# Optimization experiments

Measured on AMD Instinct MI355X. Metric: run time of the kernel, lower is better.

## Reference

```python
import jax, jax.numpy as jnp
import numpy as np

B, N, DIM, HEADS = 4, 1024, 768, 12
HIDDEN, E, TOPK = 3072, 8, 2
EPS = 1e-5  # nn.LayerNorm default


def _layernorm(x, g, b):
    mu = jnp.mean(x, axis=-1, keepdims=True)
    var = jnp.var(x, axis=-1, keepdims=True)
    return (x - mu) * jax.lax.rsqrt(var + EPS) * g + b


def setup_inputs() -> dict:
    key = jax.random.key(0)
    ks = jax.random.split(key, 10)
    s = 0.02
    return {
        "x": jax.random.normal(ks[0], (B, N, DIM), dtype=jnp.float32),
        "ln1_g": jnp.ones((DIM,), jnp.float32),
        "ln1_b": jnp.zeros((DIM,), jnp.float32),
        "qkv_w": jax.random.normal(ks[1], (3 * DIM, DIM), jnp.float32) * s,  # qkv_bias=False
        "proj_w": jax.random.normal(ks[2], (DIM, DIM), jnp.float32) * s,
        "proj_b": jnp.zeros((DIM,), jnp.float32),
        "ln2_g": jnp.ones((DIM,), jnp.float32),
        "ln2_b": jnp.zeros((DIM,), jnp.float32),
        "gate_w": jax.random.normal(ks[3], (E, DIM), jnp.float32) * s,
        "gate_b": jnp.zeros((E,), jnp.float32),
        "w1": jax.random.normal(ks[4], (E, HIDDEN, DIM), jnp.float32) * s,
        "b1": jnp.zeros((E, HIDDEN), jnp.float32),
        "w2": jax.random.normal(ks[5], (E, DIM, HIDDEN), jnp.float32) * s,
        "b2": jnp.zeros((E, DIM), jnp.float32),
    }


def reference(x, ln1_g, ln1_b, qkv_w, proj_w, proj_b, ln2_g, ln2_b,
              gate_w, gate_b, w1, b1, w2, b2):
    b, n, d = x.shape
    hd = d // HEADS
    scale = hd ** -0.5

    # ---- attention branch ----
    h = _layernorm(x, ln1_g, ln1_b)
    qkv = h @ qkv_w.T                                   # [B,N,3D]
    qkv = qkv.reshape(b, n, 3, HEADS, hd).transpose(2, 0, 3, 1, 4)
    q, k, v = qkv[0], qkv[1], qkv[2]                    # [B,H,N,hd]
    attn = jax.nn.softmax(jnp.einsum('bhnd,bhmd->bhnm', q, k) * scale, axis=-1)
    a = jnp.einsum('bhnm,bhmd->bhnd', attn, v)
    a = a.transpose(0, 2, 1, 3).reshape(b, n, d)
    a = a @ proj_w.T + proj_b
    x = x + a

    # ---- MoE branch (NaiveGate, top_k=2) ----
    h2 = _layernorm(x, ln2_g, ln2_b)
    t = h2.reshape(-1, d)                               # [T,D]
    T = t.shape[0]
    logits = t @ gate_w.T + gate_b                      # [T,E]
    top_val, top_idx = jax.lax.top_k(logits, TOPK)
    score = jax.nn.softmax(top_val, axis=-1)            # softmax over top-k logits
    # per-token combine weight for each expert, [T,E]
    cw = jnp.zeros((T, E), t.dtype).at[jnp.arange(T)[:, None], top_idx].add(score)

    out = jnp.zeros_like(t)
    for e in range(E):  # small fixed expert count; exact (no capacity drop)
        he = jax.nn.gelu(t @ w1[e].T + b1[e], approximate=False)
        ye = he @ w2[e].T + b2[e]
        out = out + cw[:, e:e + 1] * ye

    return x + out.reshape(b, n, d)
```

## Files before the change

kernel.cpp:

```cpp
#include <hip/hip_runtime.h>
#include <math.h>

typedef short s16x8 __attribute__((ext_vector_type(8)));
typedef float f32x4 __attribute__((ext_vector_type(4)));
typedef unsigned short u16x4 __attribute__((ext_vector_type(4)));
typedef unsigned short u16x8 __attribute__((ext_vector_type(8)));

#define DIM_ 768
#define HID_ 3072
#define NTOK 4096
#define CAP 9216

__device__ __forceinline__ unsigned short f2bf(float f) {
  unsigned u = __float_as_uint(f);
  u += 0x7fffu + ((u >> 16) & 1u);
  return (unsigned short)(u >> 16);
}
__device__ __forceinline__ float bf2f(unsigned short u) {
  return __uint_as_float(((unsigned)u) << 16);
}

__device__ __forceinline__ void async_cp16(const void* g, void* l) {
  __builtin_amdgcn_global_load_lds(
      (const __attribute__((address_space(1))) void*)g,
      (__attribute__((address_space(3))) void*)l, 16, 0, 0);
}

template<bool BBF>
__device__ __forceinline__ void gemm_loop(
    const unsigned short* aS0, const unsigned short* aS1,
    const void* __restrict__ Bv, int ldb,
    int kbeg, int kend, int col0,
    unsigned short* lA, unsigned short* lB,
    f32x4 acc[4][4])
{
  const int tid = threadIdx.x;
  const int lane = tid & 63;
  const int w = tid >> 6;
  const int wm = (w >> 1) << 6;
  const int wn = (w & 1) << 6;
  const int g = lane >> 4;
  const int lm = lane & 15;

  if constexpr (BBF) {
    const unsigned short* Bb = (const unsigned short*)Bv;
    const unsigned short* bS[2];
#pragma unroll
    for (int it = 0; it < 2; ++it) {
      int c = (w * 2 + it) * 64 + lane;
      int r = c >> 2, ks = ((c & 3) ^ ((r >> 1) & 3)) << 3;
      bS[it] = Bb + (size_t)(col0 + r) * ldb + ks;
    }
    auto stage = [&](int k0, int p) {
      async_cp16(aS0 + k0, lA + p * 4096 + (w * 2 + 0) * 512);
      async_cp16(bS[0] + k0, lB + p * 4096 + (w * 2 + 0) * 512);
      async_cp16(aS1 + k0, lA + p * 4096 + (w * 2 + 1) * 512);
      async_cp16(bS[1] + k0, lB + p * 4096 + (w * 2 + 1) * 512);
    };
    stage(kbeg, 0);
    int p = 0;
    for (int k0 = kbeg; k0 < kend; k0 += 32) {
      __syncthreads();
      if (k0 + 32 < kend) stage(k0 + 32, p ^ 1);
      const unsigned short* bA = lA + p * 4096;
      const unsigned short* bB = lB + p * 4096;
      s16x8 a_frag[4], b_frag[4];
#pragma unroll
      for (int mt = 0; mt < 4; ++mt) {
        int ra = wm + mt * 16 + lm;
        a_frag[mt] = *(const s16x8*)(bA + ra * 32 + ((g ^ ((ra >> 1) & 3)) << 3));
      }
#pragma unroll
      for (int nt = 0; nt < 4; ++nt) {
        int cb = wn + nt * 16 + lm;
        b_frag[nt] = *(const s16x8*)(bB + cb * 32 + ((g ^ ((cb >> 1) & 3)) << 3));
      }
#pragma unroll
      for (int mt = 0; mt < 4; ++mt)
#pragma unroll
        for (int nt = 0; nt < 4; ++nt)
          acc[mt][nt] = __builtin_amdgcn_mfma_f32_16x16x32_bf16(
              a_frag[mt], b_frag[nt], acc[mt][nt], 0, 0, 0);
      p ^= 1;
    }
  } else {
    const float* Bf = (const float*)Bv;
    for (int k0 = kbeg; k0 < kend; k0 += 32) {
      __syncthreads();
      async_cp16(aS0 + k0, lA + (w * 2 + 0) * 512);
      async_cp16(aS1 + k0, lA + (w * 2 + 1) * 512);
#pragma unroll
      for (int it = 0; it < 4; ++it) {
        int f = it * 1024 + tid * 4;
        int br = f >> 5, ke = f & 31;
        const float4 vv = *(const float4*)(Bf + (size_t)(col0 + br) * ldb + (k0 + ke));
        u16x4 pk;
        pk[0] = f2bf(vv.x); pk[1] = f2bf(vv.y); pk[2] = f2bf(vv.z); pk[3] = f2bf(vv.w);
        int ksw = (((ke >> 3) ^ ((br >> 1) & 3)) << 3) + (ke & 7);
        *(u16x4*)(lB + br * 32 + ksw) = pk;
      }
      __syncthreads();
      s16x8 a_frag[4], b_frag[4];
#pragma unroll
      for (int mt = 0; mt < 4; ++mt) {
        int ra = wm + mt * 16 + lm;
        a_frag[mt] = *(const s16x8*)(lA + ra * 32 + ((g ^ ((ra >> 1) & 3)) << 3));
      }
#pragma unroll
      for (int nt = 0; nt < 4; ++nt) {
        int cb = wn + nt * 16 + lm;
        b_frag[nt] = *(const s16x8*)(lB + cb * 32 + ((g ^ ((cb >> 1) & 3)) << 3));
      }
#pragma unroll
      for (int mt = 0; mt < 4; ++mt)
#pragma unroll
        for (int nt = 0; nt < 4; ++nt)
          acc[mt][nt] = __builtin_amdgcn_mfma_f32_16x16x32_bf16(
              a_frag[mt], b_frag[nt], acc[mt][nt], 0, 0, 0);
    }
  }
}

#define GEMM_PROLOGUE                                   \
  __shared__ unsigned short lA[8192];                   \
  __shared__ unsigned short lB[8192];                   \
  f32x4 acc[4][4];                                      \
  _Pragma("unroll") for (int a_ = 0; a_ < 4; ++a_)      \
  _Pragma("unroll") for (int b_ = 0; b_ < 4; ++b_) {    \
    acc[a_][b_][0]=0.f; acc[a_][b_][1]=0.f;             \
    acc[a_][b_][2]=0.f; acc[a_][b_][3]=0.f; }           \
  const int lane = threadIdx.x & 63;                    \
  const int w = threadIdx.x >> 6;                       \
  const int wm = (w >> 1) << 6, wn = (w & 1) << 6;      \
  const int g = lane >> 4, lm = lane & 15;

#define A_PTRS(Abase, LDA)                                            \
  const unsigned short* aS[2];                                        \
  _Pragma("unroll") for (int it_ = 0; it_ < 2; ++it_) {               \
    int c_ = (w * 2 + it_) * 64 + lane;                               \
    int r_ = c_ >> 2, ks_ = ((c_ & 3) ^ ((r_ >> 1) & 3)) << 3;        \
    aS[it_] = (Abase) + (size_t)(row0 + r_) * (LDA) + ks_;            \
  }


__global__ void k_cvtln(const float* __restrict__ s0, const float* __restrict__ s1,
                        const float* __restrict__ s2, const float* __restrict__ s3,
                        unsigned short* __restrict__ d0, unsigned short* __restrict__ d1,
                        unsigned short* __restrict__ d2, unsigned short* __restrict__ d3,
                        int ncvt,
                        const float* __restrict__ x, const float* __restrict__ gg,
                        const float* __restrict__ bb, unsigned short* __restrict__ outb)
{
  __shared__ float red[8];
  if ((int)blockIdx.x < ncvt) {
    long i = (long)(blockIdx.x * 256 + threadIdx.x) * 8;
    const float* s; unsigned short* d;
    if (i < 1769472)             { s = s0;            d = d0; }
    else if (i < 2359296)        { s = s1 - 1769472;  d = d1 - 1769472; }
    else if (i < 21233664)       { s = s2 - 2359296;  d = d2 - 2359296; }
    else                         { s = s3 - 21233664; d = d3 - 21233664; }
    float4 a = *(const float4*)(s + i);
    float4 b = *(const float4*)(s + i + 4);
    u16x8 o;
    o[0]=f2bf(a.x); o[1]=f2bf(a.y); o[2]=f2bf(a.z); o[3]=f2bf(a.w);
    o[4]=f2bf(b.x); o[5]=f2bf(b.y); o[6]=f2bf(b.z); o[7]=f2bf(b.w);
    *(u16x8*)(d + i) = o;
    return;
  }
  int t = blockIdx.x - ncvt, tid = threadIdx.x;
  const float* xr = x + (size_t)t * DIM_;
  float v0 = xr[tid], v1 = xr[tid + 256], v2 = xr[tid + 512];
  float s = v0 + v1 + v2, q = v0 * v0 + v1 * v1 + v2 * v2;
  for (int o = 32; o; o >>= 1) { s += __shfl_xor(s, o, 64); q += __shfl_xor(q, o, 64); }
  int lane = tid & 63, w = tid >> 6;
  if (!lane) { red[w] = s; red[4 + w] = q; }
  __syncthreads();
  s = red[0] + red[1] + red[2] + red[3];
  q = red[4] + red[5] + red[6] + red[7];
  float mean = s * (1.f / 768.f);
  float rstd = rsqrtf(q * (1.f / 768.f) - mean * mean + 1e-5f);
  unsigned short* orow = outb + (size_t)t * DIM_;
  orow[tid]       = f2bf((v0 - mean) * rstd * gg[tid]       + bb[tid]);
  orow[tid + 256] = f2bf((v1 - mean) * rstd * gg[tid + 256] + bb[tid + 256]);
  orow[tid + 512] = f2bf((v2 - mean) * rstd * gg[tid + 512] + bb[tid + 512]);
}

template<bool BBF>
__global__ __launch_bounds__(256, 2) void k_qkv(
    const unsigned short* __restrict__ hbf, const void* __restrict__ qkvw,
    unsigned short* __restrict__ qkvb)
{
  GEMM_PROLOGUE
  int f = blockIdx.x, xcd = f & 7, s = f >> 3;
  int cg = s / 24, rr = (s % 24) / 6, c = cg * 6 + s % 6;
  int row0 = (xcd * 4 + rr) * 128, col0 = c * 128;
  A_PTRS(hbf, DIM_)
  gemm_loop<BBF>(aS[0], aS[1], qkvw, DIM_, 0, DIM_, col0, lA, lB, acc);
#pragma unroll
  for (int mt = 0; mt < 4; ++mt)
#pragma unroll
    for (int nt = 0; nt < 4; ++nt)
#pragma unroll
      for (int i = 0; i < 4; ++i) {
        int m = row0 + wm + mt * 16 + g * 4 + i;
        int n = col0 + wn + nt * 16 + lm;
        int which = (n >= 1536) ? 2 : (n >= 768 ? 1 : 0);
        int d = n - which * 768;
        int head = d >> 6, hd = d & 63;
        int b = m >> 10, nn = m & 1023;
        int bh = b * 12 + head;
        size_t addr = (which < 2)
            ? ((size_t)which * 3145728u + (size_t)bh * 65536u + (size_t)nn * 64 + hd)
            : (6291456u + (size_t)bh * 65536u + (size_t)hd * 1024 + nn);
        qkvb[addr] = f2bf(acc[mt][nt][i]);
      }
}

__global__ __launch_bounds__(256, 2) void k_attn(
    const unsigned short* __restrict__ qkv, unsigned short* __restrict__ abuf)
{
  __shared__ unsigned short lK[2][4096];
  __shared__ unsigned short lV[2][4096];
  __shared__ unsigned short lP[4][16 * 72];
  const int tid = threadIdx.x, lane = tid & 63, w = tid >> 6;
  const int g = lane >> 4, lm = lane & 15;
  const int f = blockIdx.x, xcd = f & 7, s = f >> 3;
  const int bh = xcd * 6 + (s >> 4);
  const int qt = s & 15;
  const unsigned short* qsec = qkv + (size_t)bh * 65536u;
  const unsigned short* ksec = qkv + 3145728u + (size_t)bh * 65536u;
  const unsigned short* vsec = qkv + 6291456u + (size_t)bh * 65536u;

  s16x8 bq[2];
  {
    const unsigned short* qp = qsec + (size_t)(qt * 64 + w * 16 + lm) * 64 + g * 8;
    bq[0] = *(const s16x8*)(qp);
    bq[1] = *(const s16x8*)(qp + 32);
  }
  f32x4 oacc[4];
#pragma unroll
  for (int dt = 0; dt < 4; ++dt) { oacc[dt][0]=0.f; oacc[dt][1]=0.f; oacc[dt][2]=0.f; oacc[dt][3]=0.f; }
  float m_i = -3.0e38f, l_i = 0.f;

  auto stage = [&](int kt, int p) {
#pragma unroll
    for (int it = 0; it < 2; ++it) {
      int c = (w * 2 + it) * 64 + lane;
      int r = c >> 3, sl = (c & 7) ^ (r & 7);
      async_cp16(ksec + (size_t)(kt * 64 + r) * 64 + sl * 8, lK[p] + (w * 2 + it) * 512);
      async_cp16(vsec + (size_t)r * 1024 + kt * 64 + sl * 8, lV[p] + (w * 2 + it) * 512);
    }
  };
  stage(0, 0);
  int p = 0;
  for (int kt = 0; kt < 16; ++kt) {
    __syncthreads();
    if (kt < 15) stage(kt + 1, p ^ 1);
    f32x4 st[4];
#pragma unroll
    for (int mt = 0; mt < 4; ++mt) {
      f32x4 z; z[0]=0.f; z[1]=0.f; z[2]=0.f; z[3]=0.f;
#pragma unroll
      for (int ks = 0; ks < 2; ++ks) {
        int ra = mt * 16 + lm;
        s16x8 a = *(const s16x8*)(lK[p] + ra * 64 + (((ks * 4 + g) ^ (ra & 7)) << 3));
        z = __builtin_amdgcn_mfma_f32_16x16x32_bf16(a, bq[ks], z, 0, 0, 0);
      }
      st[mt] = z;
    }
    float mx = -3.0e38f;
#pragma unroll
    for (int mt = 0; mt < 4; ++mt) {
      st[mt] *= 0.125f;
#pragma unroll
      for (int i = 0; i < 4; ++i) mx = fmaxf(mx, st[mt][i]);
    }
    mx = fmaxf(mx, __shfl_xor(mx, 16, 64));
    mx = fmaxf(mx, __shfl_xor(mx, 32, 64));
    float mnew = fmaxf(m_i, mx);
    float alpha = expf(m_i - mnew);
    float psum = 0.f;
#pragma unroll
    for (int mt = 0; mt < 4; ++mt) {
      u16x4 pk;
#pragma unroll
      for (int i = 0; i < 4; ++i) {
        float p2 = expf(st[mt][i] - mnew);
        psum += p2;
        pk[i] = f2bf(p2);
      }
      *(u16x4*)(&lP[w][lm * 72 + mt * 16 + g * 4]) = pk;
    }
    psum += __shfl_xor(psum, 16, 64);
    psum += __shfl_xor(psum, 32, 64);
    l_i = l_i * alpha + psum;
    m_i = mnew;
    float al[4];
#pragma unroll
    for (int i = 0; i < 4; ++i) al[i] = __shfl(alpha, (lane & 48) | (g * 4 + i), 64);
#pragma unroll
    for (int dt = 0; dt < 4; ++dt) {
#pragma unroll
      for (int i = 0; i < 4; ++i) oacc[dt][i] *= al[i];
    }
#pragma unroll
    for (int ks = 0; ks < 2; ++ks) {
      s16x8 ap = *(const s16x8*)(&lP[w][lm * 72 + ks * 32 + g * 8]);
#pragma unroll
      for (int dt = 0; dt < 4; ++dt) {
        int rv = dt * 16 + lm;
        s16x8 bv = *(const s16x8*)(lV[p] + rv * 64 + (((ks * 4 + g) ^ (rv & 7)) << 3));
        oacc[dt] = __builtin_amdgcn_mfma_f32_16x16x32_bf16(ap, bv, oacc[dt], 0, 0, 0);
      }
    }
    p ^= 1;
  }
  float linv[4];
#pragma unroll
  for (int i = 0; i < 4; ++i)
    linv[i] = 1.f / __shfl(l_i, (lane & 48) | (g * 4 + i), 64);
  int b = bh / 12, head = bh % 12;
#pragma unroll
  for (int dt = 0; dt < 4; ++dt)
#pragma unroll
    for (int i = 0; i < 4; ++i) {
      int q = qt * 64 + w * 16 + g * 4 + i;
      int col = head * 64 + dt * 16 + lm;
      abuf[(size_t)(b * 1024 + q) * DIM_ + col] = f2bf(oacc[dt][i] * linv[i]);
    }
}

template<bool BBF>
__global__ __launch_bounds__(256, 2) void k_proj(
    const unsigned short* __restrict__ abuf, const void* __restrict__ projw,
    const float* __restrict__ projb, const float* __restrict__ x,
    float* __restrict__ x1)
{
  GEMM_PROLOGUE
  int row0 = blockIdx.x * 128, col0 = blockIdx.y * 128;
  A_PTRS(abuf, DIM_)
  gemm_loop<BBF>(aS[0], aS[1], projw, DIM_, 0, DIM_, col0, lA, lB, acc);
#pragma unroll
  for (int mt = 0; mt < 4; ++mt)
#pragma unroll
    for (int nt = 0; nt < 4; ++nt)
#pragma unroll
      for (int i = 0; i < 4; ++i) {
        int m = row0 + wm + mt * 16 + g * 4 + i;
        int n = col0 + wn + nt * 16 + lm;
        size_t idx = (size_t)m * DIM_ + n;
        x1[idx] = acc[mt][nt][i] + projb[n] + x[idx];
      }
}

template<bool BBF>
__global__ __launch_bounds__(256, 2) void k_ffn1(
    const unsigned short* __restrict__ h2, const void* __restrict__ w1,
    const float* __restrict__ b1, const int* __restrict__ off,
    const int* __restrict__ tok_of, const unsigned short* __restrict__ zrow,
    unsigned short* __restrict__ hidden)
{
  int f = blockIdx.x, xcd = f & 7, s = f >> 3;
  int cg = s / 72, rr = (s % 72) >> 3, c = cg * 8 + (s & 7);
  int row0 = (xcd * 9 + rr) * 128, col0 = c * 128;
  if (row0 >= off[8]) return;
  int e = 0;
  while (!(row0 >= off[e] && row0 < off[e + 1])) ++e;
  GEMM_PROLOGUE
  const unsigned short* aS[2];
#pragma unroll
  for (int it = 0; it < 2; ++it) {
    int cc = (w * 2 + it) * 64 + lane;
    int r = cc >> 2, ks = ((cc & 3) ^ ((r >> 1) & 3)) << 3;
    int tk = tok_of[row0 + r];
    const unsigned short* rp = (tk >= 0) ? (h2 + (size_t)tk * DIM_) : zrow;
    aS[it] = rp + ks;
  }
  const char* Bp = (const char*)w1 + (size_t)e * HID_ * DIM_ * (BBF ? 2 : 4);
  gemm_loop<BBF>(aS[0], aS[1], Bp, DIM_, 0, DIM_, col0, lA, lB, acc);
#pragma unroll
  for (int mt = 0; mt < 4; ++mt)
#pragma unroll
    for (int nt = 0; nt < 4; ++nt)
#pragma unroll
      for (int i = 0; i < 4; ++i) {
        int m = row0 + wm + mt * 16 + g * 4 + i;
        int n = col0 + wn + nt * 16 + lm;
        float v = acc[mt][nt][i] + b1[e * HID_ + n];
        float ge = 0.5f * v * (1.f + erff(v * 0.70710678118654752f));
        hidden[(size_t)m * HID_ + n] = f2bf(ge);
      }
}

template<bool BBF>
__global__ __launch_bounds__(256, 2) void k_ffn2(
    const unsigned short* __restrict__ hidden, const void* __restrict__ w2,
    const float* __restrict__ b2, const int* __restrict__ off,
    unsigned short* __restrict__ ye0, unsigned short* __restrict__ ye1)
{
  int f = blockIdx.x, xcd = f & 7, s = f >> 3;
  int cg = s / 54, rem = s % 54;
  int rr = rem / 6, kk = (rem % 6) / 3, c = cg * 3 + rem % 3;
  int row0 = (xcd * 9 + rr) * 128, col0 = c * 128;
  if (row0 >= off[8]) return;
  int e = 0;
  while (!(row0 >= off[e] && row0 < off[e + 1])) ++e;
  GEMM_PROLOGUE
  A_PTRS(hidden, HID_)
  const char* Bp = (const char*)w2 + (size_t)e * DIM_ * HID_ * (BBF ? 2 : 4);
  gemm_loop<BBF>(aS[0], aS[1], Bp, HID_, kk * 1536, kk * 1536 + 1536, col0, lA, lB, acc);
  unsigned short* yh = kk ? ye1 : ye0;
#pragma unroll
  for (int mt = 0; mt < 4; ++mt)
#pragma unroll
    for (int nt = 0; nt < 4; ++nt)
#pragma unroll
      for (int i = 0; i < 4; ++i) {
        int m = row0 + wm + mt * 16 + g * 4 + i;
        int n = col0 + wn + nt * 16 + lm;
        float v = acc[mt][nt][i] + (kk ? 0.f : b2[e * DIM_ + n]);
        yh[(size_t)m * DIM_ + n] = f2bf(v);
      }
}

__global__ __launch_bounds__(256) void k_ln2gate(
    const float* __restrict__ x1, const float* __restrict__ gg,
    const float* __restrict__ bb, const float* __restrict__ gw,
    const float* __restrict__ gb, unsigned short* __restrict__ h2,
    int* __restrict__ topidx, float* __restrict__ tops)
{
  int t = blockIdx.x, tid = threadIdx.x;
  const float* xr = x1 + (size_t)t * DIM_;
  float v0 = xr[tid], v1 = xr[tid + 256], v2 = xr[tid + 512];
  float s = v0 + v1 + v2, q = v0 * v0 + v1 * v1 + v2 * v2;
  for (int o = 32; o; o >>= 1) { s += __shfl_xor(s, o, 64); q += __shfl_xor(q, o, 64); }
  __shared__ float red[8];
  __shared__ float part[32];
  int lane = tid & 63, w = tid >> 6;
  if (!lane) { red[w] = s; red[4 + w] = q; }
  __syncthreads();
  s = red[0] + red[1] + red[2] + red[3];
  q = red[4] + red[5] + red[6] + red[7];
  float mean = s * (1.f / 768.f);
  float rstd = rsqrtf(q * (1.f / 768.f) - mean * mean + 1e-5f);
  float y0 = (v0 - mean) * rstd * gg[tid]       + bb[tid];
  float y1 = (v1 - mean) * rstd * gg[tid + 256] + bb[tid + 256];
  float y2 = (v2 - mean) * rstd * gg[tid + 512] + bb[tid + 512];
  unsigned short* hrow = h2 + (size_t)t * DIM_;
  hrow[tid] = f2bf(y0); hrow[tid + 256] = f2bf(y1); hrow[tid + 512] = f2bf(y2);
#pragma unroll
  for (int e = 0; e < 8; ++e) {
    float p = y0 * gw[e * DIM_ + tid] + y1 * gw[e * DIM_ + tid + 256] + y2 * gw[e * DIM_ + tid + 512];
    for (int o = 32; o; o >>= 1) p += __shfl_xor(p, o, 64);
    if (!lane) part[e * 4 + w] = p;
  }
  __syncthreads();
  if (tid == 0) {
    float lg[8];
#pragma unroll
    for (int e = 0; e < 8; ++e)
      lg[e] = part[e * 4] + part[e * 4 + 1] + part[e * 4 + 2] + part[e * 4 + 3] + gb[e];
    int i0 = 0; float b0 = lg[0];
#pragma unroll
    for (int e = 1; e < 8; ++e) if (lg[e] > b0) { b0 = lg[e]; i0 = e; }
    int i1 = (i0 == 0) ? 1 : 0; float b1v = lg[i1];
#pragma unroll
    for (int e = 0; e < 8; ++e)
      if (e != i0 && lg[e] > b1v) { b1v = lg[e]; i1 = e; }
    float e1 = expf(b1v - b0);
    float s0 = 1.f / (1.f + e1);
    topidx[t * 2] = i0; topidx[t * 2 + 1] = i1;
    tops[t * 2] = s0;  tops[t * 2 + 1] = e1 / (1.f + e1);
  }
}

__global__ __launch_bounds__(1024) void k_route(
    const int* __restrict__ topidx, int* __restrict__ pos_of, int* __restrict__ off,
    int* __restrict__ tok_of, unsigned short* __restrict__ zrow)
{
  __shared__ int scnt[8], soff[9], sfill[8];
  int tid = threadIdx.x;
  if (tid < 8) { scnt[tid] = 0; sfill[tid] = 0; }
  if (tid < 384) ((unsigned*)zrow)[tid] = 0;
  for (int j = tid; j < CAP; j += 1024) tok_of[j] = -1;
  __syncthreads();
#pragma unroll
  for (int j = 0; j < 8; ++j)
    atomicAdd(&scnt[topidx[tid + j * 1024]], 1);
  __syncthreads();
  if (tid == 0) {
    int a = 0;
    for (int e = 0; e < 8; ++e) { soff[e] = a; off[e] = a; a += (scnt[e] + 127) & ~127; }
    soff[8] = a; off[8] = a;
  }
  __syncthreads();
#pragma unroll
  for (int j = 0; j < 8; ++j) {
    int i = tid + j * 1024;
    int e = topidx[i];
    int p = soff[e] + atomicAdd(&sfill[e], 1);
    pos_of[i] = p;
    tok_of[p] = i >> 1;
  }
}

__global__ void k_combine(const float* __restrict__ x1,
                          const unsigned short* __restrict__ y0h,
                          const unsigned short* __restrict__ y1h,
                          const int* __restrict__ pos_of, const float* __restrict__ tops,
                          float* __restrict__ out) {
  int t = blockIdx.x, tid = threadIdx.x;
  int p0 = pos_of[t * 2], p1 = pos_of[t * 2 + 1];
  float s0 = tops[t * 2], s1 = tops[t * 2 + 1];
  const float* xr = x1 + (size_t)t * DIM_;
  const unsigned short* a0 = y0h + (size_t)p0 * DIM_;
  const unsigned short* a1 = y1h + (size_t)p0 * DIM_;
  const unsigned short* b0 = y0h + (size_t)p1 * DIM_;
  const unsigned short* b1 = y1h + (size_t)p1 * DIM_;
  float* orow = out + (size_t)t * DIM_;
#pragma unroll
  for (int j = 0; j < 3; ++j) {
    int col = tid + j * 256;
    float ya = bf2f(a0[col]) + bf2f(a1[col]);
    float yb = bf2f(b0[col]) + bf2f(b1[col]);
    orow[col] = xr[col] + s0 * ya + s1 * yb;
  }
}

extern "C" void kernel_launch(void* const* d_in, const int* in_sizes, int n_in,
                              void* d_out, int out_size, void* d_ws, size_t ws_size,
                              hipStream_t stream) {
  const float* x     = (const float*)d_in[0];
  const float* ln1g  = (const float*)d_in[1];
  const float* ln1b  = (const float*)d_in[2];
  const float* qkvw  = (const float*)d_in[3];
  const float* projw = (const float*)d_in[4];
  const float* projb = (const float*)d_in[5];
  const float* ln2g  = (const float*)d_in[6];
  const float* ln2b  = (const float*)d_in[7];
  const float* gw    = (const float*)d_in[8];
  const float* gb    = (const float*)d_in[9];
  const float* w1    = (const float*)d_in[10];
  const float* b1    = (const float*)d_in[11];
  const float* w2    = (const float*)d_in[12];
  const float* b2    = (const float*)d_in[13];
  float* out = (float*)d_out;

  char* base = (char*)d_ws;
  unsigned short* hbf    = (unsigned short*)(base + 0);
  unsigned short* qkvb   = (unsigned short*)(base + 6291456);
  unsigned short* abuf   = (unsigned short*)(base + 25165824);
  float*          x1     = (float*)(base + 31457280);
  unsigned short* hidden = (unsigned short*)(base + 44040192);
  unsigned short* ye0    = (unsigned short*)(base + 100663296);
  unsigned short* ye1    = (unsigned short*)(base + 114819072);

  const size_t FULL_NEED = 209190912;
  const bool full = ws_size >= FULL_NEED;
  unsigned short *wqkvbf, *wprojbf, *w1bf = nullptr, *w2bf = nullptr;
  if (full) {
    wqkvbf  = (unsigned short*)(base + 128974848);
    wprojbf = (unsigned short*)(base + 132513792);
    w1bf    = (unsigned short*)(base + 133693440);
    w2bf    = (unsigned short*)(base + 171442176);
  } else {
    wqkvbf  = (unsigned short*)(base + 44040192);
    wprojbf = (unsigned short*)(base + 44040192 + 3538944);
  }
  char* small = base + 25165824;
  int*   topidx = (int*)small;
  float* tops   = (float*)(small + 32768);
  int*   pos_of = (int*)(small + 65536);
  int*   off    = (int*)(small + 98304);
  int*   tok_of = (int*)(small + 98368);
  unsigned short* zrow = (unsigned short*)(small + 135232);
  unsigned short* h2 = hbf;

  int ncvt = full ? 19584 : 1152;
  k_cvtln<<<ncvt + NTOK, 256, 0, stream>>>(qkvw, projw, w1, w2,
                                           wqkvbf, wprojbf, w1bf, w2bf,
                                           ncvt, x, ln1g, ln1b, hbf);
  k_qkv<true><<<576, 256, 0, stream>>>(hbf, wqkvbf, qkvb);
  k_attn<<<768, 256, 0, stream>>>(qkvb, abuf);
  k_proj<true><<<dim3(32, 6), 256, 0, stream>>>(abuf, wprojbf, projb, x, x1);
  k_ln2gate<<<NTOK, 256, 0, stream>>>(x1, ln2g, ln2b, gw, gb, h2, topidx, tops);
  k_route<<<1, 1024, 0, stream>>>(topidx, pos_of, off, tok_of, zrow);
  if (full) {
    k_ffn1<true><<<1728, 256, 0, stream>>>(h2, w1bf, b1, off, tok_of, zrow, hidden);
    k_ffn2<true><<<864, 256, 0, stream>>>(hidden, w2bf, b2, off, ye0, ye1);
  } else {
    k_ffn1<false><<<1728, 256, 0, stream>>>(h2, w1, b1, off, tok_of, zrow, hidden);
    k_ffn2<false><<<864, 256, 0, stream>>>(hidden, w2, b2, off, ye0, ye1);
  }
  k_combine<<<NTOK, 256, 0, stream>>>(x1, ye0, ye1, pos_of, tops, out);
}
```

Baseline: 481.0 us.

## Fuse MoE combine into ffn2 via atomics and overlap weight conversion with QKV

```diff
diff --git a/kernel.cpp b/kernel.cpp
--- a/kernel.cpp
+++ b/kernel.cpp
@@ -24,6 +24,16 @@
   __builtin_amdgcn_global_load_lds(
       (const __attribute__((address_space(1))) void*)g,
       (__attribute__((address_space(3))) void*)l, 16, 0, 0);
+}
+
+__device__ __forceinline__ void cvt2048(const float* __restrict__ s,
+                                        unsigned short* __restrict__ d, long i) {
+  float4 a = *(const float4*)(s + i);
+  float4 b = *(const float4*)(s + i + 4);
+  u16x8 o;
+  o[0]=f2bf(a.x); o[1]=f2bf(a.y); o[2]=f2bf(a.z); o[3]=f2bf(a.w);
+  o[4]=f2bf(b.x); o[5]=f2bf(b.y); o[6]=f2bf(b.z); o[7]=f2bf(b.w);
+  *(u16x8*)(d + i) = o;
 }
 
 template<bool BBF>
@@ -144,30 +154,18 @@
 
 
 __global__ void k_cvtln(const float* __restrict__ s0, const float* __restrict__ s1,
-                        const float* __restrict__ s2, const float* __restrict__ s3,
                         unsigned short* __restrict__ d0, unsigned short* __restrict__ d1,
-                        unsigned short* __restrict__ d2, unsigned short* __restrict__ d3,
-                        int ncvt,
                         const float* __restrict__ x, const float* __restrict__ gg,
                         const float* __restrict__ bb, unsigned short* __restrict__ outb)
 {
   __shared__ float red[8];
-  if ((int)blockIdx.x < ncvt) {
+  if ((int)blockIdx.x < 1152) {
     long i = (long)(blockIdx.x * 256 + threadIdx.x) * 8;
-    const float* s; unsigned short* d;
-    if (i < 1769472)             { s = s0;            d = d0; }
-    else if (i < 2359296)        { s = s1 - 1769472;  d = d1 - 1769472; }
-    else if (i < 21233664)       { s = s2 - 2359296;  d = d2 - 2359296; }
-    else                         { s = s3 - 21233664; d = d3 - 21233664; }
-    float4 a = *(const float4*)(s + i);
-    float4 b = *(const float4*)(s + i + 4);
-    u16x8 o;
-    o[0]=f2bf(a.x); o[1]=f2bf(a.y); o[2]=f2bf(a.z); o[3]=f2bf(a.w);
-    o[4]=f2bf(b.x); o[5]=f2bf(b.y); o[6]=f2bf(b.z); o[7]=f2bf(b.w);
-    *(u16x8*)(d + i) = o;
+    if (i < 1769472) cvt2048(s0, d0, i);
+    else             cvt2048(s1 - 1769472, d1 - 1769472, i);
     return;
   }
-  int t = blockIdx.x - ncvt, tid = threadIdx.x;
+  int t = blockIdx.x - 1152, tid = threadIdx.x;
   const float* xr = x + (size_t)t * DIM_;
   float v0 = xr[tid], v1 = xr[tid + 256], v2 = xr[tid + 512];
   float s = v0 + v1 + v2, q = v0 * v0 + v1 * v1 + v2 * v2;
@@ -185,17 +183,27 @@
   orow[tid + 512] = f2bf((v2 - mean) * rstd * gg[tid + 512] + bb[tid + 512]);
 }
 
-template<bool BBF>
-__global__ __launch_bounds__(256, 2) void k_qkv(
+template<bool FULL>
+__global__ __launch_bounds__(256, 4) void k_qkvcvt(
     const unsigned short* __restrict__ hbf, const void* __restrict__ qkvw,
-    unsigned short* __restrict__ qkvb)
+    unsigned short* __restrict__ qkvb,
+    const float* __restrict__ w1f, const float* __restrict__ w2f,
+    unsigned short* __restrict__ w1bf, unsigned short* __restrict__ w2bf)
 {
   GEMM_PROLOGUE
+  if constexpr (FULL) {
+    if ((int)blockIdx.x >= 576) {
+      int c2 = blockIdx.x - 576;
+      if (c2 < 9216) cvt2048(w1f, w1bf, (long)c2 * 2048 + threadIdx.x * 8);
+      else           cvt2048(w2f, w2bf, (long)(c2 - 9216) * 2048 + threadIdx.x * 8);
+      return;
+    }
+  }
   int f = blockIdx.x, xcd = f & 7, s = f >> 3;
   int cg = s / 24, rr = (s % 24) / 6, c = cg * 6 + s % 6;
   int row0 = (xcd * 4 + rr) * 128, col0 = c * 128;
   A_PTRS(hbf, DIM_)
-  gemm_loop<BBF>(aS[0], aS[1], qkvw, DIM_, 0, DIM_, col0, lA, lB, acc);
+  gemm_loop<true>(aS[0], aS[1], qkvw, DIM_, 0, DIM_, col0, lA, lB, acc);
 #pragma unroll
   for (int mt = 0; mt < 4; ++mt)
 #pragma unroll
@@ -330,8 +338,7 @@
     }
 }
 
-template<bool BBF>
-__global__ __launch_bounds__(256, 2) void k_proj(
+__global__ __launch_bounds__(256, 4) void k_proj(
     const unsigned short* __restrict__ abuf, const void* __restrict__ projw,
     const float* __restrict__ projb, const float* __restrict__ x,
     float* __restrict__ x1)
@@ -339,7 +346,7 @@
   GEMM_PROLOGUE
   int row0 = blockIdx.x * 128, col0 = blockIdx.y * 128;
   A_PTRS(abuf, DIM_)
-  gemm_loop<BBF>(aS[0], aS[1], projw, DIM_, 0, DIM_, col0, lA, lB, acc);
+  gemm_loop<true>(aS[0], aS[1], projw, DIM_, 0, DIM_, col0, lA, lB, acc);
 #pragma unroll
   for (int mt = 0; mt < 4; ++mt)
 #pragma unroll
@@ -354,7 +361,7 @@
 }
 
 template<bool BBF>
-__global__ __launch_bounds__(256, 2) void k_ffn1(
+__global__ __launch_bounds__(256, 4) void k_ffn1(
     const unsigned short* __restrict__ h2, const void* __restrict__ w1,
     const float* __restrict__ b1, const int* __restrict__ off,
     const int* __restrict__ tok_of, const unsigned short* __restrict__ zrow,
@@ -393,10 +400,11 @@
 }
 
 template<bool BBF>
-__global__ __launch_bounds__(256, 2) void k_ffn2(
+__global__ __launch_bounds__(256, 4) void k_ffn2(
     const unsigned short* __restrict__ hidden, const void* __restrict__ w2,
     const float* __restrict__ b2, const int* __restrict__ off,
-    unsigned short* __restrict__ ye0, unsigned short* __restrict__ ye1)
+    const int* __restrict__ tok_of, const float* __restrict__ cw_of,
+    float* __restrict__ out)
 {
   int f = blockIdx.x, xcd = f & 7, s = f >> 3;
   int cg = s / 54, rem = s % 54;
@@ -409,29 +417,35 @@
   A_PTRS(hidden, HID_)
   const char* Bp = (const char*)w2 + (size_t)e * DIM_ * HID_ * (BBF ? 2 : 4);
   gemm_loop<BBF>(aS[0], aS[1], Bp, HID_, kk * 1536, kk * 1536 + 1536, col0, lA, lB, acc);
-  unsigned short* yh = kk ? ye1 : ye0;
 #pragma unroll
   for (int mt = 0; mt < 4; ++mt)
 #pragma unroll
-    for (int nt = 0; nt < 4; ++nt)
-#pragma unroll
-      for (int i = 0; i < 4; ++i) {
-        int m = row0 + wm + mt * 16 + g * 4 + i;
+    for (int i = 0; i < 4; ++i) {
+      int m = row0 + wm + mt * 16 + g * 4 + i;
+      int tok = tok_of[m];
+      if (tok < 0) continue;
+      float cw = cw_of[m];
+      float* orow = out + (size_t)tok * DIM_;
+#pragma unroll
+      for (int nt = 0; nt < 4; ++nt) {
         int n = col0 + wn + nt * 16 + lm;
         float v = acc[mt][nt][i] + (kk ? 0.f : b2[e * DIM_ + n]);
-        yh[(size_t)m * DIM_ + n] = f2bf(v);
-      }
+        atomicAdd(orow + n, cw * v);
+      }
+    }
 }
 
 __global__ __launch_bounds__(256) void k_ln2gate(
     const float* __restrict__ x1, const float* __restrict__ gg,
     const float* __restrict__ bb, const float* __restrict__ gw,
     const float* __restrict__ gb, unsigned short* __restrict__ h2,
-    int* __restrict__ topidx, float* __restrict__ tops)
+    int* __restrict__ topidx, float* __restrict__ tops, float* __restrict__ out)
 {
   int t = blockIdx.x, tid = threadIdx.x;
   const float* xr = x1 + (size_t)t * DIM_;
   float v0 = xr[tid], v1 = xr[tid + 256], v2 = xr[tid + 512];
+  float* orow = out + (size_t)t * DIM_;
+  orow[tid] = v0; orow[tid + 256] = v1; orow[tid + 512] = v2;
   float s = v0 + v1 + v2, q = v0 * v0 + v1 * v1 + v2 * v2;
   for (int o = 32; o; o >>= 1) { s += __shfl_xor(s, o, 64); q += __shfl_xor(q, o, 64); }
   __shared__ float red[8];
@@ -475,8 +489,9 @@
 }
 
 __global__ __launch_bounds__(1024) void k_route(
-    const int* __restrict__ topidx, int* __restrict__ pos_of, int* __restrict__ off,
-    int* __restrict__ tok_of, unsigned short* __restrict__ zrow)
+    const int* __restrict__ topidx, const float* __restrict__ tops,
+    int* __restrict__ off, int* __restrict__ tok_of, float* __restrict__ cw_of,
+    unsigned short* __restrict__ zrow)
 {
   __shared__ int scnt[8], soff[9], sfill[8];
   int tid = threadIdx.x;
@@ -499,31 +514,8 @@
     int i = tid + j * 1024;
     int e = topidx[i];
     int p = soff[e] + atomicAdd(&sfill[e], 1);
-    pos_of[i] = p;
     tok_of[p] = i >> 1;
-  }
-}
-
-__global__ void k_combine(const float* __restrict__ x1,
-                          const unsigned short* __restrict__ y0h,
-                          const unsigned short* __restrict__ y1h,
-                          const int* __restrict__ pos_of, const float* __restrict__ tops,
-                          float* __restrict__ out) {
-  int t = blockIdx.x, tid = threadIdx.x;
-  int p0 = pos_of[t * 2], p1 = pos_of[t * 2 + 1];
-  float s0 = tops[t * 2], s1 = tops[t * 2 + 1];
-  const float* xr = x1 + (size_t)t * DIM_;
-  const unsigned short* a0 = y0h + (size_t)p0 * DIM_;
-  const unsigned short* a1 = y1h + (size_t)p0 * DIM_;
-  const unsigned short* b0 = y0h + (size_t)p1 * DIM_;
-  const unsigned short* b1 = y1h + (size_t)p1 * DIM_;
-  float* orow = out + (size_t)t * DIM_;
-#pragma unroll
-  for (int j = 0; j < 3; ++j) {
-    int col = tid + j * 256;
-    float ya = bf2f(a0[col]) + bf2f(a1[col]);
-    float yb = bf2f(b0[col]) + bf2f(b1[col]);
-    orow[col] = xr[col] + s0 * ya + s1 * yb;
+    cw_of[p] = tops[i];
   }
 }
 
@@ -552,8 +544,6 @@
   unsigned short* abuf   = (unsigned short*)(base + 25165824);
   float*          x1     = (float*)(base + 31457280);
   unsigned short* hidden = (unsigned short*)(base + 44040192);
-  unsigned short* ye0    = (unsigned short*)(base + 100663296);
-  unsigned short* ye1    = (unsigned short*)(base + 114819072);
 
   const size_t FULL_NEED = 209190912;
   const bool full = ws_size >= FULL_NEED;
@@ -570,27 +560,29 @@
   char* small = base + 25165824;
   int*   topidx = (int*)small;
   float* tops   = (float*)(small + 32768);
-  int*   pos_of = (int*)(small + 65536);
-  int*   off    = (int*)(small + 98304);
-  int*   tok_of = (int*)(small + 98368);
-  unsigned short* zrow = (unsigned short*)(small + 135232);
+  int*   off    = (int*)(small + 65536);
+  int*   tok_of = (int*)(small + 65600);
+  float* cw_of  = (float*)(small + 102464);
+  unsigned short* zrow = (unsigned short*)(small + 139392);
   unsigned short* h2 = hbf;
 
-  int ncvt = full ? 19584 : 1152;
-  k_cvtln<<<ncvt + NTOK, 256, 0, stream>>>(qkvw, projw, w1, w2,
-                                           wqkvbf, wprojbf, w1bf, w2bf,
-                                           ncvt, x, ln1g, ln1b, hbf);
-  k_qkv<true><<<576, 256, 0, stream>>>(hbf, wqkvbf, qkvb);
+  k_cvtln<<<1152 + NTOK, 256, 0, stream>>>(qkvw, projw, wqkvbf, wprojbf,
+                                           x, ln1g, ln1b, hbf);
+  if (full)
+    k_qkvcvt<true><<<576 + 18432, 256, 0, stream>>>(hbf, wqkvbf, qkvb,
+                                                    w1, w2, w1bf, w2bf);
+  else
+    k_qkvcvt<false><<<576, 256, 0, stream>>>(hbf, wqkvbf, qkvb,
+                                             nullptr, nullptr, nullptr, nullptr);
   k_attn<<<768, 256, 0, stream>>>(qkvb, abuf);
-  k_proj<true><<<dim3(32, 6), 256, 0, stream>>>(abuf, wprojbf, projb, x, x1);
-  k_ln2gate<<<NTOK, 256, 0, stream>>>(x1, ln2g, ln2b, gw, gb, h2, topidx, tops);
-  k_route<<<1, 1024, 0, stream>>>(topidx, pos_of, off, tok_of, zrow);
+  k_proj<<<dim3(32, 6), 256, 0, stream>>>(abuf, wprojbf, projb, x, x1);
+  k_ln2gate<<<NTOK, 256, 0, stream>>>(x1, ln2g, ln2b, gw, gb, h2, topidx, tops, out);
+  k_route<<<1, 1024, 0, stream>>>(topidx, tops, off, tok_of, cw_of, zrow);
   if (full) {
     k_ffn1<true><<<1728, 256, 0, stream>>>(h2, w1bf, b1, off, tok_of, zrow, hidden);
-    k_ffn2<true><<<864, 256, 0, stream>>>(hidden, w2bf, b2, off, ye0, ye1);
+    k_ffn2<true><<<864, 256, 0, stream>>>(hidden, w2bf, b2, off, tok_of, cw_of, out);
   } else {
     k_ffn1<false><<<1728, 256, 0, stream>>>(h2, w1, b1, off, tok_of, zrow, hidden);
-    k_ffn2<false><<<864, 256, 0, stream>>>(hidden, w2, b2, off, ye0, ye1);
-  }
-  k_combine<<<NTOK, 256, 0, stream>>>(x1, ye0, ye1, pos_of, tops, out);
-}
+    k_ffn2<false><<<864, 256, 0, stream>>>(hidden, w2, b2, off, tok_of, cw_of, out);
+  }
+}
```

After: 503.2 us. +4.6%, slower.

## Move expert weight conversion into QKV GEMM launch and raise occupancy bounds

Applied to the files above, without the earlier changes.

```diff
diff --git a/kernel.cpp b/kernel.cpp
--- a/kernel.cpp
+++ b/kernel.cpp
@@ -24,6 +24,16 @@
   __builtin_amdgcn_global_load_lds(
       (const __attribute__((address_space(1))) void*)g,
       (__attribute__((address_space(3))) void*)l, 16, 0, 0);
+}
+
+__device__ __forceinline__ void cvt2048(const float* __restrict__ s,
+                                        unsigned short* __restrict__ d, long i) {
+  float4 a = *(const float4*)(s + i);
+  float4 b = *(const float4*)(s + i + 4);
+  u16x8 o;
+  o[0]=f2bf(a.x); o[1]=f2bf(a.y); o[2]=f2bf(a.z); o[3]=f2bf(a.w);
+  o[4]=f2bf(b.x); o[5]=f2bf(b.y); o[6]=f2bf(b.z); o[7]=f2bf(b.w);
+  *(u16x8*)(d + i) = o;
 }
 
 template<bool BBF>
@@ -144,30 +154,18 @@
 
 
 __global__ void k_cvtln(const float* __restrict__ s0, const float* __restrict__ s1,
-                        const float* __restrict__ s2, const float* __restrict__ s3,
                         unsigned short* __restrict__ d0, unsigned short* __restrict__ d1,
-                        unsigned short* __restrict__ d2, unsigned short* __restrict__ d3,
-                        int ncvt,
                         const float* __restrict__ x, const float* __restrict__ gg,
                         const float* __restrict__ bb, unsigned short* __restrict__ outb)
 {
   __shared__ float red[8];
-  if ((int)blockIdx.x < ncvt) {
+  if ((int)blockIdx.x < 1152) {
     long i = (long)(blockIdx.x * 256 + threadIdx.x) * 8;
-    const float* s; unsigned short* d;
-    if (i < 1769472)             { s = s0;            d = d0; }
-    else if (i < 2359296)        { s = s1 - 1769472;  d = d1 - 1769472; }
-    else if (i < 21233664)       { s = s2 - 2359296;  d = d2 - 2359296; }
-    else                         { s = s3 - 21233664; d = d3 - 21233664; }
-    float4 a = *(const float4*)(s + i);
-    float4 b = *(const float4*)(s + i + 4);
-    u16x8 o;
-    o[0]=f2bf(a.x); o[1]=f2bf(a.y); o[2]=f2bf(a.z); o[3]=f2bf(a.w);
-    o[4]=f2bf(b.x); o[5]=f2bf(b.y); o[6]=f2bf(b.z); o[7]=f2bf(b.w);
-    *(u16x8*)(d + i) = o;
+    if (i < 1769472) cvt2048(s0, d0, i);
+    else             cvt2048(s1 - 1769472, d1 - 1769472, i);
     return;
   }
-  int t = blockIdx.x - ncvt, tid = threadIdx.x;
+  int t = blockIdx.x - 1152, tid = threadIdx.x;
   const float* xr = x + (size_t)t * DIM_;
   float v0 = xr[tid], v1 = xr[tid + 256], v2 = xr[tid + 512];
   float s = v0 + v1 + v2, q = v0 * v0 + v1 * v1 + v2 * v2;
@@ -185,17 +183,27 @@
   orow[tid + 512] = f2bf((v2 - mean) * rstd * gg[tid + 512] + bb[tid + 512]);
 }
 
-template<bool BBF>
-__global__ __launch_bounds__(256, 2) void k_qkv(
+template<bool FULL>
+__global__ __launch_bounds__(256, 4) void k_qkvcvt(
     const unsigned short* __restrict__ hbf, const void* __restrict__ qkvw,
-    unsigned short* __restrict__ qkvb)
+    unsigned short* __restrict__ qkvb,
+    const float* __restrict__ w1f, const float* __restrict__ w2f,
+    unsigned short* __restrict__ w1bf, unsigned short* __restrict__ w2bf)
 {
   GEMM_PROLOGUE
+  if constexpr (FULL) {
+    if ((int)blockIdx.x >= 576) {
+      int c2 = blockIdx.x - 576;
+      if (c2 < 9216) cvt2048(w1f, w1bf, (long)c2 * 2048 + threadIdx.x * 8);
+      else           cvt2048(w2f, w2bf, (long)(c2 - 9216) * 2048 + threadIdx.x * 8);
+      return;
+    }
+  }
   int f = blockIdx.x, xcd = f & 7, s = f >> 3;
   int cg = s / 24, rr = (s % 24) / 6, c = cg * 6 + s % 6;
   int row0 = (xcd * 4 + rr) * 128, col0 = c * 128;
   A_PTRS(hbf, DIM_)
-  gemm_loop<BBF>(aS[0], aS[1], qkvw, DIM_, 0, DIM_, col0, lA, lB, acc);
+  gemm_loop<true>(aS[0], aS[1], qkvw, DIM_, 0, DIM_, col0, lA, lB, acc);
 #pragma unroll
   for (int mt = 0; mt < 4; ++mt)
 #pragma unroll
@@ -330,8 +338,7 @@
     }
 }
 
-template<bool BBF>
-__global__ __launch_bounds__(256, 2) void k_proj(
+__global__ __launch_bounds__(256, 4) void k_proj(
     const unsigned short* __restrict__ abuf, const void* __restrict__ projw,
     const float* __restrict__ projb, const float* __restrict__ x,
     float* __restrict__ x1)
@@ -339,7 +346,7 @@
   GEMM_PROLOGUE
   int row0 = blockIdx.x * 128, col0 = blockIdx.y * 128;
   A_PTRS(abuf, DIM_)
-  gemm_loop<BBF>(aS[0], aS[1], projw, DIM_, 0, DIM_, col0, lA, lB, acc);
+  gemm_loop<true>(aS[0], aS[1], projw, DIM_, 0, DIM_, col0, lA, lB, acc);
 #pragma unroll
   for (int mt = 0; mt < 4; ++mt)
 #pragma unroll
@@ -354,7 +361,7 @@
 }
 
 template<bool BBF>
-__global__ __launch_bounds__(256, 2) void k_ffn1(
+__global__ __launch_bounds__(256, 4) void k_ffn1(
     const unsigned short* __restrict__ h2, const void* __restrict__ w1,
     const float* __restrict__ b1, const int* __restrict__ off,
     const int* __restrict__ tok_of, const unsigned short* __restrict__ zrow,
@@ -393,7 +400,7 @@
 }
 
 template<bool BBF>
-__global__ __launch_bounds__(256, 2) void k_ffn2(
+__global__ __launch_bounds__(256, 4) void k_ffn2(
     const unsigned short* __restrict__ hidden, const void* __restrict__ w2,
     const float* __restrict__ b2, const int* __restrict__ off,
     unsigned short* __restrict__ ye0, unsigned short* __restrict__ ye1)
@@ -576,13 +583,16 @@
   unsigned short* zrow = (unsigned short*)(small + 135232);
   unsigned short* h2 = hbf;
 
-  int ncvt = full ? 19584 : 1152;
-  k_cvtln<<<ncvt + NTOK, 256, 0, stream>>>(qkvw, projw, w1, w2,
-                                           wqkvbf, wprojbf, w1bf, w2bf,
-                                           ncvt, x, ln1g, ln1b, hbf);
-  k_qkv<true><<<576, 256, 0, stream>>>(hbf, wqkvbf, qkvb);
+  k_cvtln<<<1152 + NTOK, 256, 0, stream>>>(qkvw, projw, wqkvbf, wprojbf,
+                                           x, ln1g, ln1b, hbf);
+  if (full)
+    k_qkvcvt<true><<<576 + 18432, 256, 0, stream>>>(hbf, wqkvbf, qkvb,
+                                                    w1, w2, w1bf, w2bf);
+  else
+    k_qkvcvt<false><<<576, 256, 0, stream>>>(hbf, wqkvbf, qkvb,
+                                             nullptr, nullptr, nullptr, nullptr);
   k_attn<<<768, 256, 0, stream>>>(qkvb, abuf);
-  k_proj<true><<<dim3(32, 6), 256, 0, stream>>>(abuf, wprojbf, projb, x, x1);
+  k_proj<<<dim3(32, 6), 256, 0, stream>>>(abuf, wprojbf, projb, x, x1);
   k_ln2gate<<<NTOK, 256, 0, stream>>>(x1, ln2g, ln2b, gw, gb, h2, topidx, tops);
   k_route<<<1, 1024, 0, stream>>>(topidx, pos_of, off, tok_of, zrow);
   if (full) {
```

New measurement: 477.7 us. Within noise of the previous version (-0.7%).
